# Optimization experiments

Hardware: AMD Instinct MI355X
Metric: run time of the kernel (lower is better)

## Reference

```python
import jax, jax.numpy as jnp
import numpy as np

N = 50000
E = 1600000
DX = 128
DH = 128
DY = 64
NEG_SLOPE = 0.0  # in_neg_slope; LeakyReLU slope in GAT attention


def _init(key, shape, fan_in):
    return jax.random.normal(key, shape, dtype=jnp.float32) / np.sqrt(fan_in)


def setup_inputs() -> dict:
    key = jax.random.key(0)
    ks = jax.random.split(key, 12)
    node_x = jax.random.normal(ks[0], (N, DX), dtype=jnp.float32)
    edge_index = jax.random.randint(ks[1], (2, E), 0, N, dtype=jnp.int32)
    return {
        "node_x": node_x,
        "edge_index": edge_index,
        # GATConv layer 1 (DX -> DH, heads=1)
        "W1": _init(ks[2], (DX, DH), DX),
        "att_src1": _init(ks[3], (DH,), DH),
        "att_dst1": _init(ks[4], (DH,), DH),
        "b1": jnp.zeros((DH,), dtype=jnp.float32),
        # GATConv layer 2 (DH -> DH)
        "W2": _init(ks[5], (DH, DH), DH),
        "att_src2": _init(ks[6], (DH,), DH),
        "att_dst2": _init(ks[7], (DH,), DH),
        "b2": jnp.zeros((DH,), dtype=jnp.float32),
        # output Linear (DH -> DY)
        "W_out": _init(ks[8], (DH, DY), DH),
        "b_out": jnp.zeros((DY,), dtype=jnp.float32),
    }


def _gat_conv(x, src, dst, W, att_src, att_dst, bias, n):
    # h: [N, DH] transformed features
    h = x @ W
    # per-edge attention logits: a_src . h_j + a_dst . h_i
    e = (h @ att_src)[src] + (h @ att_dst)[dst]          # [E']
    e = jnp.where(e > 0, e, NEG_SLOPE * e)               # LeakyReLU
    # segment softmax over incoming edges of each destination node
    m = jax.lax.stop_gradient(jax.ops.segment_max(e, dst, num_segments=n))
    ex = jnp.exp(e - m[dst])
    denom = jax.ops.segment_sum(ex, dst, num_segments=n)
    alpha = ex / denom[dst]                              # [E']
    # scatter-add weighted source features to destinations
    out = jax.ops.segment_sum(h[src] * alpha[:, None], dst, num_segments=n)
    return out + bias


def reference(node_x, edge_index, W1, att_src1, att_dst1, b1,
              W2, att_src2, att_dst2, b2, W_out, b_out):
    n = node_x.shape[0]
    src, dst = edge_index[0], edge_index[1]
    # PyG GATConv default add_self_loops=True
    loop = jnp.arange(n, dtype=src.dtype)
    src = jnp.concatenate([src, loop])
    dst = jnp.concatenate([dst, loop])
    x1 = jax.nn.relu(_gat_conv(node_x, src, dst, W1, att_src1, att_dst1, b1, n))
    x2 = _gat_conv(x1, src, dst, W2, att_src2, att_dst2, b2, n)
    return x2 @ W_out + b_out
```

## Files before the change

### kernel.cpp

```cpp
#include <hip/hip_runtime.h>
#include <hip/hip_fp16.h>

typedef unsigned short u16;
typedef unsigned int   u32;
typedef _Float16 f16;
typedef __attribute__((ext_vector_type(8))) f16 f16x8;
typedef __attribute__((ext_vector_type(2))) f16 h2;
typedef __attribute__((ext_vector_type(4))) float f32x4;

#define NN 50000
#define EE 1600000
#define DD 128
#define DYY 64
#define NB 196
#define EPB 8192
#define GB 196
#define MAXD 160
#define NTILE 3125
#define GMM 782

__device__ __forceinline__ u16 f2h(float f){
  union { f16 h; u16 u; } x; x.h = (f16)f; return x.u;
}
__device__ __forceinline__ float wave_sum(float v){
  #pragma unroll
  for (int s = 32; s; s >>= 1) v += __shfl_xor(v, s, 64);
  return v;
}

__device__ __forceinline__ void wfrag_one(const float* __restrict__ W, u16* __restrict__ Wf,
                                          int nct, int s){
  int lane = s & 63;
  int t  = (s >> 6) % nct;
  int ks = (s >> 6) / nct;
  int q = lane >> 4, n = lane & 15;
  int N = nct * 16;
  u16 tmp[8];
  #pragma unroll
  for (int j = 0; j < 8; ++j)
    tmp[j] = f2h(W[(ks * 32 + q * 8 + j) * N + t * 16 + n]);
  *(uint4*)(Wf + (size_t)s * 8) = *(const uint4*)tmp;
}

__global__ __launch_bounds__(256) void kA_prep(const int* __restrict__ dst, int* __restrict__ hist2d,
                                               const float* __restrict__ W1, const float* __restrict__ W2,
                                               const float* __restrict__ Wo,
                                               u16* __restrict__ Wf1, u16* __restrict__ Wf2,
                                               u16* __restrict__ Wfo){
  int b = blockIdx.x, tid = threadIdx.x;
  if (b < GB){
    __shared__ int hist[256];
    hist[tid] = 0;
    __syncthreads();
    int e0 = b * EPB, e1 = min(e0 + EPB, EE);
    for (int e = e0 + tid; e < e1; e += 256) atomicAdd(&hist[dst[e] >> 8], 1);
    __syncthreads();
    hist2d[b * 256 + tid] = hist[tid];
  } else if (b < 204) wfrag_one(W1, Wf1, 8, (b - 196) * 256 + tid);
  else if (b < 212)   wfrag_one(W2, Wf2, 8, (b - 204) * 256 + tid);
  else                wfrag_one(Wo, Wfo, 4, (b - 212) * 256 + tid);
}

__device__ __forceinline__ void gemm_tile(const void* __restrict__ X, int xf32,
                                          const u16* __restrict__ Wf, u16* __restrict__ Hout,
                                          const float* __restrict__ as, const float* __restrict__ ad,
                                          float* __restrict__ Sv, float* __restrict__ Dv,
                                          int blk, int tid, uint4* Wl){
  const uint4* Wg = (const uint4*)Wf;
  #pragma unroll
  for (int i = 0; i < 8; ++i) Wl[tid + 256 * i] = Wg[tid + 256 * i];
  __syncthreads();
  int wv = tid >> 6, lane = tid & 63;
  int rtile = blk * 4 + wv;
  if (rtile >= NTILE) return;
  int q = lane >> 4, n = lane & 15;
  int arow = rtile * 16 + n;
  f32x4 acc[8];
  #pragma unroll
  for (int t = 0; t < 8; ++t) acc[t] = (f32x4){0.f, 0.f, 0.f, 0.f};
  union F8 { uint4 u; f16x8 v; f16 h[8]; };
  #pragma unroll
  for (int ks = 0; ks < 4; ++ks){
    int kb = ks * 32 + q * 8;
    F8 a;
    if (!xf32){
      a.u = *(const uint4*)((const u16*)X + (size_t)arow * DD + kb);
    } else {
      const float* xp = (const float*)X + (size_t)arow * DD + kb;
      float4 f0 = *(const float4*)xp;
      float4 f1 = *(const float4*)(xp + 4);
      a.h[0] = (f16)f0.x; a.h[1] = (f16)f0.y; a.h[2] = (f16)f0.z; a.h[3] = (f16)f0.w;
      a.h[4] = (f16)f1.x; a.h[5] = (f16)f1.y; a.h[6] = (f16)f1.z; a.h[7] = (f16)f1.w;
    }
    #pragma unroll
    for (int t = 0; t < 8; ++t){
      F8 b; b.u = Wl[(ks * 8 + t) * 64 + lane];
      acc[t] = __builtin_amdgcn_mfma_f32_16x16x32_f16(a.v, b.v, acc[t], 0, 0, 0);
    }
  }
  float ps[4] = {0, 0, 0, 0}, pd[4] = {0, 0, 0, 0};
  #pragma unroll
  for (int t = 0; t < 8; ++t){
    float a_s = as[t * 16 + n];
    float a_d = ad[t * 16 + n];
    #pragma unroll
    for (int rg = 0; rg < 4; ++rg){
      ps[rg] += acc[t][rg] * a_s;
      pd[rg] += acc[t][rg] * a_d;
    }
  }
  #pragma unroll
  for (int rg = 0; rg < 4; ++rg){
    #pragma unroll
    for (int s = 1; s < 16; s <<= 1){
      ps[rg] += __shfl_xor(ps[rg], s, 64);
      pd[rg] += __shfl_xor(pd[rg], s, 64);
    }
  }
  #pragma unroll
  for (int rg = 0; rg < 4; ++rg){
    int grow = rtile * 16 + q * 4 + rg;
    if (n == 0){ Sv[grow] = ps[rg]; Dv[grow] = pd[rg]; }
    #pragma unroll
    for (int t = 0; t < 8; ++t)
      Hout[(size_t)grow * DD + t * 16 + n] = f2h(acc[t][rg]);
  }
}

__global__ __launch_bounds__(256) void kBC(const int* __restrict__ src, const int* __restrict__ dst,
                                           const int* __restrict__ hist2d,
                                           int* __restrict__ btot, int* __restrict__ bbase,
                                           u32* __restrict__ buf,
                                           const float* __restrict__ X0, const u16* __restrict__ Wf1,
                                           u16* __restrict__ Hbf,
                                           const float* __restrict__ as1, const float* __restrict__ ad1,
                                           float* __restrict__ Sv, float* __restrict__ Dv){
  __shared__ __align__(16) uint4 Wl[2048];
  int b = blockIdx.x, tid = threadIdx.x;
  if (b < GB){
    int* lcur = (int*)Wl;
    int* sd   = ((int*)Wl) + 256;
    int c = b;
    int pre = 0, tot = 0;
    for (int cc = 0; cc < GB; ++cc){
      int v = hist2d[cc * 256 + tid];
      if (cc < c) pre += v;
      tot += v;
    }
    sd[tid] = tot;
    __syncthreads();
    for (int o = 1; o < 256; o <<= 1){
      int t = (tid >= o) ? sd[tid - o] : 0;
      __syncthreads();
      sd[tid] += t;
      __syncthreads();
    }
    int bb = sd[tid] - tot;
    if (c == 0){ btot[tid] = tot; bbase[tid] = bb; }
    lcur[tid] = bb + pre;
    __syncthreads();
    int e0 = c * EPB, e1 = min(e0 + EPB, EE);
    for (int e = e0 + tid; e < e1; e += 256){
      int d = dst[e];
      int pos = atomicAdd(&lcur[d >> 8], 1);
      buf[pos] = (u32)src[e] | ((u32)(d & 255) << 16);
    }
  } else {
    gemm_tile(X0, 1, Wf1, Hbf, as1, ad1, Sv, Dv, b - GB, tid, Wl);
  }
}

__global__ __launch_bounds__(256) void kD_finalize(const u32* __restrict__ buf,
                                                   const int* __restrict__ btot, const int* __restrict__ bbase,
                                                   int* __restrict__ offs, int* __restrict__ cnt,
                                                   u16* __restrict__ srcs){
  __shared__ int dh[256];
  __shared__ int sd[256];
  __shared__ int dcur[256];
  int tid = threadIdx.x, b = blockIdx.x;
  int n = btot[b], base = bbase[b];
  dh[tid] = 0;
  __syncthreads();
  for (int i = tid; i < n; i += 256) atomicAdd(&dh[(buf[base + i] >> 16) & 255], 1);
  __syncthreads();
  int v = dh[tid];
  sd[tid] = v;
  __syncthreads();
  for (int o = 1; o < 256; o <<= 1){
    int t = (tid >= o) ? sd[tid - o] : 0;
    __syncthreads();
    sd[tid] += t;
    __syncthreads();
  }
  int excl = sd[tid] - v;
  dcur[tid] = base + excl;
  int d = (b << 8) + tid;
  if (d < NN){ offs[d] = base + excl; cnt[d] = v; }
  __syncthreads();
  for (int i = tid; i < n; i += 256){
    u32 u = buf[base + i];
    int pos = atomicAdd(&dcur[(u >> 16) & 255], 1);
    srcs[pos] = (u16)(u & 0xffffu);
  }
}

__global__ __launch_bounds__(256) void k_agg(const u16* __restrict__ H,
                                             const float* __restrict__ Sv, const float* __restrict__ Dv,
                                             const int* __restrict__ offs, const int* __restrict__ cnt,
                                             const u16* __restrict__ srcs,
                                             const float* __restrict__ bias,
                                             u16* __restrict__ Xout, int do_relu){
  __shared__ int   s_i[4][MAXD];
  __shared__ float s_w[4][MAXD];
  int gid = blockIdx.x * blockDim.x + threadIdx.x;
  int wid = gid >> 6, lane = gid & 63;
  int wv = threadIdx.x >> 6;
  if (wid >= NN) return;
  int off = offs[wid], c = cnt[wid];
  float dvw = Dv[wid];
  float wself = __expf(fmaxf(Sv[wid] + dvw, 0.f));
  int cf = min(c, MAXD);
  float dl = 0.f;
  for (int j = lane; j < c; j += 64){
    int sidx = (int)srcs[off + j];
    float wgt = __expf(fmaxf(Sv[sidx] + dvw, 0.f));
    if (j < MAXD){ s_i[wv][j] = sidx; s_w[wv][j] = wgt; }
    dl += wgt;
  }
  float inv = 1.f / (wave_sum(dl) + wself);
  for (int j = lane; j < cf; j += 64) s_w[wv][j] *= inv;
  int grp = lane >> 4, cg = lane & 15;
  const u32* H32 = (const u32*)H;
  union F8 { uint4 u; h2 p[4]; };
  h2 acc2[4] = {(h2){0,0},(h2){0,0},(h2){0,0},(h2){0,0}};
  if (grp == 0){
    F8 r; r.u = *(const uint4*)(H32 + (size_t)wid * 64 + cg * 4);
    f16 wh = (f16)(wself * inv); h2 w2 = {wh, wh};
    #pragma unroll
    for (int i = 0; i < 4; ++i) acc2[i] = r.p[i] * w2;
  }
  for (int base = 0; base < cf; base += 4){
    int j = base + grp;
    float wgt = 0.f; int sidx = 0;
    if (j < cf){ wgt = s_w[wv][j]; sidx = s_i[wv][j]; }
    f16 wh = (f16)wgt; h2 w2 = {wh, wh};
    F8 r; r.u = *(const uint4*)(H32 + (size_t)sidx * 64 + cg * 4);
    #pragma unroll
    for (int i = 0; i < 4; ++i) acc2[i] += r.p[i] * w2;
  }
  for (int base = MAXD; base < c; base += 4){
    int j = base + grp;
    bool valid = j < c;
    int sidx = valid ? (int)srcs[off + j] : 0;
    float wgt = valid ? __expf(fmaxf(Sv[sidx] + dvw, 0.f)) * inv : 0.f;
    f16 wh = (f16)wgt; h2 w2 = {wh, wh};
    F8 r; r.u = *(const uint4*)(H32 + (size_t)sidx * 64 + cg * 4);
    #pragma unroll
    for (int i = 0; i < 4; ++i) acc2[i] += r.p[i] * w2;
  }
  union FU { h2 v; float f; };
  #pragma unroll
  for (int i = 0; i < 4; ++i){
    FU a; a.v = acc2[i];
    FU o1; o1.f = __shfl_xor(a.f, 16, 64); a.v = a.v + o1.v;
    FU o2; o2.f = __shfl_xor(a.f, 32, 64); a.v = a.v + o2.v;
    acc2[i] = a.v;
  }
  if (grp == 0){
    uint4 pk;
    u32* pkp = (u32*)&pk;
    #pragma unroll
    for (int qq = 0; qq < 4; ++qq){
      float o0 = (float)acc2[qq].x + bias[cg * 8 + 2 * qq];
      float o1 = (float)acc2[qq].y + bias[cg * 8 + 2 * qq + 1];
      if (do_relu){ o0 = fmaxf(o0, 0.f); o1 = fmaxf(o1, 0.f); }
      pkp[qq] = ((u32)f2h(o1) << 16) | (u32)f2h(o0);
    }
    *(uint4*)((u32*)Xout + (size_t)wid * 64 + cg * 4) = pk;
  }
}

__global__ __launch_bounds__(256) void k_gemm2(const u16* __restrict__ X, const u16* __restrict__ Wf,
                                               u16* __restrict__ Hout,
                                               const float* __restrict__ as, const float* __restrict__ ad,
                                               float* __restrict__ Sv, float* __restrict__ Dv){
  __shared__ __align__(16) uint4 Wl[2048];
  gemm_tile(X, 0, Wf, Hout, as, ad, Sv, Dv, blockIdx.x, threadIdx.x, Wl);
}

__global__ __launch_bounds__(256) void k_out(const u16* __restrict__ X,
                                             const u16* __restrict__ Wfo,
                                             const float* __restrict__ bias,
                                             float* __restrict__ out){
  __shared__ __align__(16) uint4 Wl[1024];
  int tid = threadIdx.x;
  const uint4* Wg = (const uint4*)Wfo;
  #pragma unroll
  for (int i = 0; i < 4; ++i) Wl[tid + 256 * i] = Wg[tid + 256 * i];
  __syncthreads();
  int wv = tid >> 6, lane = tid & 63;
  int rtile = blockIdx.x * 4 + wv;
  if (rtile >= NTILE) return;
  int q = lane >> 4, n = lane & 15;
  int arow = rtile * 16 + n;
  f32x4 acc[4];
  #pragma unroll
  for (int t = 0; t < 4; ++t) acc[t] = (f32x4){0.f, 0.f, 0.f, 0.f};
  union F8 { uint4 u; f16x8 v; };
  #pragma unroll
  for (int ks = 0; ks < 4; ++ks){
    F8 a; a.u = *(const uint4*)(X + (size_t)arow * DD + ks * 32 + q * 8);
    #pragma unroll
    for (int t = 0; t < 4; ++t){
      F8 b; b.u = Wl[(ks * 4 + t) * 64 + lane];
      acc[t] = __builtin_amdgcn_mfma_f32_16x16x32_f16(a.v, b.v, acc[t], 0, 0, 0);
    }
  }
  float bo[4];
  #pragma unroll
  for (int t = 0; t < 4; ++t) bo[t] = bias[t * 16 + n];
  #pragma unroll
  for (int rg = 0; rg < 4; ++rg){
    int grow = rtile * 16 + q * 4 + rg;
    #pragma unroll
    for (int t = 0; t < 4; ++t)
      out[(size_t)grow * DYY + t * 16 + n] = acc[t][rg] + bo[t];
  }
}

extern "C" void kernel_launch(void* const* d_in, const int* in_sizes, int n_in,
                              void* d_out, int out_size, void* d_ws, size_t ws_size,
                              hipStream_t stream) {
  const float* node_x = (const float*)d_in[0];
  const int* ei   = (const int*)d_in[1];
  const int* srcp = ei;
  const int* dstp = ei + EE;
  const float* W1  = (const float*)d_in[2];
  const float* as1 = (const float*)d_in[3];
  const float* ad1 = (const float*)d_in[4];
  const float* b1  = (const float*)d_in[5];
  const float* W2  = (const float*)d_in[6];
  const float* as2 = (const float*)d_in[7];
  const float* ad2 = (const float*)d_in[8];
  const float* b2  = (const float*)d_in[9];
  const float* Wo  = (const float*)d_in[10];
  const float* bo  = (const float*)d_in[11];

  char* w = (char*)d_ws;
  u16*   Hbf   = (u16*)w;   w += (size_t)NN * DD * 2;
  u16*   Abf   = (u16*)w;   w += (size_t)NN * DD * 2;
  u32*   buf   = (u32*)Abf;
  float* Sv    = (float*)w; w += (size_t)NN * 4;
  float* Dv    = (float*)w; w += (size_t)NN * 4;
  int*   cnt   = (int*)w;   w += (size_t)NN * 4;
  int*   offs  = (int*)w;   w += (size_t)NN * 4;
  int*   btot  = (int*)w;   w += 1024;
  int*   bbase = (int*)w;   w += 1024;
  int*   hist2d = (int*)w;  w += GB * 256 * 4;
  u16*   srcs  = (u16*)w;   w += (size_t)EE * 2;
  u16*   Wf1   = (u16*)w;   w += 32768;
  u16*   Wf2   = (u16*)w;   w += 32768;
  u16*   Wfo   = (u16*)w;   w += 16384;

  const int TB = 256;
  const int gWav = (NN * 64) / TB;

  kA_prep    <<<216,      TB, 0, stream>>>(dstp, hist2d, W1, W2, Wo, Wf1, Wf2, Wfo);
  kBC        <<<GB + GMM, TB, 0, stream>>>(srcp, dstp, hist2d, btot, bbase, buf,
                                           node_x, Wf1, Hbf, as1, ad1, Sv, Dv);
  kD_finalize<<<NB,       TB, 0, stream>>>(buf, btot, bbase, offs, cnt, srcs);

  k_agg  <<<gWav, TB, 0, stream>>>(Hbf, Sv, Dv, offs, cnt, srcs, b1, Abf, 1);
  k_gemm2<<<GMM,  TB, 0, stream>>>(Abf, Wf2, Hbf, as2, ad2, Sv, Dv);
  k_agg  <<<gWav, TB, 0, stream>>>(Hbf, Sv, Dv, offs, cnt, srcs, b2, Abf, 0);
  k_out  <<<GMM,  TB, 0, stream>>>(Abf, Wfo, bo, (float*)d_out);
}
```

Baseline: 285.4 us.

## Fuse neighbor aggregation with following GEMM via LDS-staged 16-row tiles

```diff
diff --git a/kernel.cpp b/kernel.cpp
--- a/kernel.cpp
+++ b/kernel.cpp
@@ -18,6 +18,7 @@
 #define MAXD 160
 #define NTILE 3125
 #define GMM 782
+#define XST 144
 
 __device__ __forceinline__ u16 f2h(float f){
   union { f16 h; u16 u; } x; x.h = (f16)f; return x.u;
@@ -61,7 +62,7 @@
   else                wfrag_one(Wo, Wfo, 4, (b - 212) * 256 + tid);
 }
 
-__device__ __forceinline__ void gemm_tile(const void* __restrict__ X, int xf32,
+__device__ __forceinline__ void gemm_tile(const float* __restrict__ X,
                                           const u16* __restrict__ Wf, u16* __restrict__ Hout,
                                           const float* __restrict__ as, const float* __restrict__ ad,
                                           float* __restrict__ Sv, float* __restrict__ Dv,
@@ -82,16 +83,12 @@
   #pragma unroll
   for (int ks = 0; ks < 4; ++ks){
     int kb = ks * 32 + q * 8;
+    const float* xp = X + (size_t)arow * DD + kb;
+    float4 f0 = *(const float4*)xp;
+    float4 f1 = *(const float4*)(xp + 4);
     F8 a;
-    if (!xf32){
-      a.u = *(const uint4*)((const u16*)X + (size_t)arow * DD + kb);
-    } else {
-      const float* xp = (const float*)X + (size_t)arow * DD + kb;
-      float4 f0 = *(const float4*)xp;
-      float4 f1 = *(const float4*)(xp + 4);
-      a.h[0] = (f16)f0.x; a.h[1] = (f16)f0.y; a.h[2] = (f16)f0.z; a.h[3] = (f16)f0.w;
-      a.h[4] = (f16)f1.x; a.h[5] = (f16)f1.y; a.h[6] = (f16)f1.z; a.h[7] = (f16)f1.w;
-    }
+    a.h[0] = (f16)f0.x; a.h[1] = (f16)f0.y; a.h[2] = (f16)f0.z; a.h[3] = (f16)f0.w;
+    a.h[4] = (f16)f1.x; a.h[5] = (f16)f1.y; a.h[6] = (f16)f1.z; a.h[7] = (f16)f1.w;
     #pragma unroll
     for (int t = 0; t < 8; ++t){
       F8 b; b.u = Wl[(ks * 8 + t) * 64 + lane];
@@ -132,9 +129,9 @@
                                            int* __restrict__ btot, int* __restrict__ bbase,
                                            u32* __restrict__ buf,
                                            const float* __restrict__ X0, const u16* __restrict__ Wf1,
-                                           u16* __restrict__ Hbf,
+                                           u16* __restrict__ Hbf1,
                                            const float* __restrict__ as1, const float* __restrict__ ad1,
-                                           float* __restrict__ Sv, float* __restrict__ Dv){
+                                           float* __restrict__ Sv1, float* __restrict__ Dv1){
   __shared__ __align__(16) uint4 Wl[2048];
   int b = blockIdx.x, tid = threadIdx.x;
   if (b < GB){
@@ -166,7 +163,7 @@
       buf[pos] = (u32)src[e] | ((u32)(d & 255) << 16);
     }
   } else {
-    gemm_tile(X0, 1, Wf1, Hbf, as1, ad1, Sv, Dv, b - GB, tid, Wl);
+    gemm_tile(X0, Wf1, Hbf1, as1, ad1, Sv1, Dv1, b - GB, tid, Wl);
   }
 }
 
@@ -204,18 +201,11 @@
   }
 }
 
-__global__ __launch_bounds__(256) void k_agg(const u16* __restrict__ H,
-                                             const float* __restrict__ Sv, const float* __restrict__ Dv,
-                                             const int* __restrict__ offs, const int* __restrict__ cnt,
-                                             const u16* __restrict__ srcs,
-                                             const float* __restrict__ bias,
-                                             u16* __restrict__ Xout, int do_relu){
-  __shared__ int   s_i[4][MAXD];
-  __shared__ float s_w[4][MAXD];
-  int gid = blockIdx.x * blockDim.x + threadIdx.x;
-  int wid = gid >> 6, lane = gid & 63;
-  int wv = threadIdx.x >> 6;
-  if (wid >= NN) return;
+__device__ void agg_node_lds(const u16* __restrict__ H, const float* __restrict__ Sv,
+                             const float* __restrict__ Dv, const int* __restrict__ offs,
+                             const int* __restrict__ cnt, const u16* __restrict__ srcs,
+                             const float* __restrict__ bias, u16* __restrict__ xrow,
+                             int do_relu, int wid, int lane, int* si, float* sw){
   int off = offs[wid], c = cnt[wid];
   float dvw = Dv[wid];
   float wself = __expf(fmaxf(Sv[wid] + dvw, 0.f));
@@ -224,17 +214,17 @@
   for (int j = lane; j < c; j += 64){
     int sidx = (int)srcs[off + j];
     float wgt = __expf(fmaxf(Sv[sidx] + dvw, 0.f));
-    if (j < MAXD){ s_i[wv][j] = sidx; s_w[wv][j] = wgt; }
+    if (j < MAXD){ si[j] = sidx; sw[j] = wgt; }
     dl += wgt;
   }
   float inv = 1.f / (wave_sum(dl) + wself);
-  for (int j = lane; j < cf; j += 64) s_w[wv][j] *= inv;
-  int grp = lane >> 4, cg = lane & 15;
+  for (int j = lane; j < cf; j += 64) sw[j] *= inv;
+  int grp = lane >> 4, cg_ = lane & 15;
   const u32* H32 = (const u32*)H;
   union F8 { uint4 u; h2 p[4]; };
   h2 acc2[4] = {(h2){0,0},(h2){0,0},(h2){0,0},(h2){0,0}};
   if (grp == 0){
-    F8 r; r.u = *(const uint4*)(H32 + (size_t)wid * 64 + cg * 4);
+    F8 r; r.u = *(const uint4*)(H32 + (size_t)wid * 64 + cg_ * 4);
     f16 wh = (f16)(wself * inv); h2 w2 = {wh, wh};
     #pragma unroll
     for (int i = 0; i < 4; ++i) acc2[i] = r.p[i] * w2;
@@ -242,9 +232,9 @@
   for (int base = 0; base < cf; base += 4){
     int j = base + grp;
     float wgt = 0.f; int sidx = 0;
-    if (j < cf){ wgt = s_w[wv][j]; sidx = s_i[wv][j]; }
+    if (j < cf){ wgt = sw[j]; sidx = si[j]; }
     f16 wh = (f16)wgt; h2 w2 = {wh, wh};
-    F8 r; r.u = *(const uint4*)(H32 + (size_t)sidx * 64 + cg * 4);
+    F8 r; r.u = *(const uint4*)(H32 + (size_t)sidx * 64 + cg_ * 4);
     #pragma unroll
     for (int i = 0; i < 4; ++i) acc2[i] += r.p[i] * w2;
   }
@@ -254,7 +244,7 @@
     int sidx = valid ? (int)srcs[off + j] : 0;
     float wgt = valid ? __expf(fmaxf(Sv[sidx] + dvw, 0.f)) * inv : 0.f;
     f16 wh = (f16)wgt; h2 w2 = {wh, wh};
-    F8 r; r.u = *(const uint4*)(H32 + (size_t)sidx * 64 + cg * 4);
+    F8 r; r.u = *(const uint4*)(H32 + (size_t)sidx * 64 + cg_ * 4);
     #pragma unroll
     for (int i = 0; i < 4; ++i) acc2[i] += r.p[i] * w2;
   }
@@ -271,60 +261,121 @@
     u32* pkp = (u32*)&pk;
     #pragma unroll
     for (int qq = 0; qq < 4; ++qq){
-      float o0 = (float)acc2[qq].x + bias[cg * 8 + 2 * qq];
-      float o1 = (float)acc2[qq].y + bias[cg * 8 + 2 * qq + 1];
+      float o0 = (float)acc2[qq].x + bias[cg_ * 8 + 2 * qq];
+      float o1 = (float)acc2[qq].y + bias[cg_ * 8 + 2 * qq + 1];
       if (do_relu){ o0 = fmaxf(o0, 0.f); o1 = fmaxf(o1, 0.f); }
       pkp[qq] = ((u32)f2h(o1) << 16) | (u32)f2h(o0);
     }
-    *(uint4*)((u32*)Xout + (size_t)wid * 64 + cg * 4) = pk;
-  }
-}
-
-__global__ __launch_bounds__(256) void k_gemm2(const u16* __restrict__ X, const u16* __restrict__ Wf,
-                                               u16* __restrict__ Hout,
-                                               const float* __restrict__ as, const float* __restrict__ ad,
-                                               float* __restrict__ Sv, float* __restrict__ Dv){
-  __shared__ __align__(16) uint4 Wl[2048];
-  gemm_tile(X, 0, Wf, Hout, as, ad, Sv, Dv, blockIdx.x, threadIdx.x, Wl);
-}
-
-__global__ __launch_bounds__(256) void k_out(const u16* __restrict__ X,
-                                             const u16* __restrict__ Wfo,
-                                             const float* __restrict__ bias,
-                                             float* __restrict__ out){
-  __shared__ __align__(16) uint4 Wl[1024];
-  int tid = threadIdx.x;
-  const uint4* Wg = (const uint4*)Wfo;
-  #pragma unroll
-  for (int i = 0; i < 4; ++i) Wl[tid + 256 * i] = Wg[tid + 256 * i];
-  __syncthreads();
-  int wv = tid >> 6, lane = tid & 63;
-  int rtile = blockIdx.x * 4 + wv;
-  if (rtile >= NTILE) return;
+    *(uint4*)(xrow + cg_ * 8) = pk;
+  }
+}
+
+__global__ __launch_bounds__(256) void kE(const u16* __restrict__ Hbf1,
+                                          const float* __restrict__ Sv1, const float* __restrict__ Dv1,
+                                          const int* __restrict__ offs, const int* __restrict__ cnt,
+                                          const u16* __restrict__ srcs, const float* __restrict__ b1,
+                                          const u16* __restrict__ Wf2,
+                                          const float* __restrict__ as2, const float* __restrict__ ad2,
+                                          u16* __restrict__ Hbf2,
+                                          float* __restrict__ Sv2, float* __restrict__ Dv2){
+  __shared__ __align__(16) u16 Xs[16 * XST];
+  __shared__ int   s_i[4][MAXD];
+  __shared__ float s_w[4][MAXD];
+  __shared__ float svp[16], dvp[16];
+  int tid = threadIdx.x, wv = tid >> 6, lane = tid & 63;
+  int rtile = blockIdx.x;
+  if (tid < 16){ svp[tid] = 0.f; dvp[tid] = 0.f; }
+  #pragma unroll
+  for (int k = 0; k < 4; ++k){
+    int r = wv * 4 + k;
+    agg_node_lds(Hbf1, Sv1, Dv1, offs, cnt, srcs, b1, Xs + r * XST, 1,
+                 rtile * 16 + r, lane, s_i[wv], s_w[wv]);
+  }
+  __syncthreads();
+  const uint4* Wg = (const uint4*)Wf2;
   int q = lane >> 4, n = lane & 15;
-  int arow = rtile * 16 + n;
-  f32x4 acc[4];
-  #pragma unroll
-  for (int t = 0; t < 4; ++t) acc[t] = (f32x4){0.f, 0.f, 0.f, 0.f};
+  f32x4 acc[2] = {(f32x4){0.f,0.f,0.f,0.f}, (f32x4){0.f,0.f,0.f,0.f}};
   union F8 { uint4 u; f16x8 v; };
   #pragma unroll
   for (int ks = 0; ks < 4; ++ks){
-    F8 a; a.u = *(const uint4*)(X + (size_t)arow * DD + ks * 32 + q * 8);
-    #pragma unroll
-    for (int t = 0; t < 4; ++t){
-      F8 b; b.u = Wl[(ks * 4 + t) * 64 + lane];
-      acc[t] = __builtin_amdgcn_mfma_f32_16x16x32_f16(a.v, b.v, acc[t], 0, 0, 0);
-    }
-  }
-  float bo[4];
-  #pragma unroll
-  for (int t = 0; t < 4; ++t) bo[t] = bias[t * 16 + n];
+    F8 a; a.u = *(const uint4*)((const char*)Xs + n * (XST * 2) + ks * 64 + q * 16);
+    #pragma unroll
+    for (int tt = 0; tt < 2; ++tt){
+      F8 b; b.u = Wg[(ks * 8 + wv * 2 + tt) * 64 + lane];
+      acc[tt] = __builtin_amdgcn_mfma_f32_16x16x32_f16(a.v, b.v, acc[tt], 0, 0, 0);
+    }
+  }
+  float ps[4] = {0, 0, 0, 0}, pd[4] = {0, 0, 0, 0};
+  #pragma unroll
+  for (int tt = 0; tt < 2; ++tt){
+    int t = wv * 2 + tt;
+    float a_s = as2[t * 16 + n];
+    float a_d = ad2[t * 16 + n];
+    #pragma unroll
+    for (int rg = 0; rg < 4; ++rg){
+      ps[rg] += acc[tt][rg] * a_s;
+      pd[rg] += acc[tt][rg] * a_d;
+    }
+  }
+  #pragma unroll
+  for (int rg = 0; rg < 4; ++rg){
+    #pragma unroll
+    for (int s = 1; s < 16; s <<= 1){
+      ps[rg] += __shfl_xor(ps[rg], s, 64);
+      pd[rg] += __shfl_xor(pd[rg], s, 64);
+    }
+  }
+  if (n == 0){
+    #pragma unroll
+    for (int rg = 0; rg < 4; ++rg){
+      atomicAdd(&svp[q * 4 + rg], ps[rg]);
+      atomicAdd(&dvp[q * 4 + rg], pd[rg]);
+    }
+  }
   #pragma unroll
   for (int rg = 0; rg < 4; ++rg){
     int grow = rtile * 16 + q * 4 + rg;
     #pragma unroll
-    for (int t = 0; t < 4; ++t)
-      out[(size_t)grow * DYY + t * 16 + n] = acc[t][rg] + bo[t];
+    for (int tt = 0; tt < 2; ++tt)
+      Hbf2[(size_t)grow * DD + (wv * 2 + tt) * 16 + n] = f2h(acc[tt][rg]);
+  }
+  __syncthreads();
+  if (tid < 16){ Sv2[rtile * 16 + tid] = svp[tid]; Dv2[rtile * 16 + tid] = dvp[tid]; }
+}
+
+__global__ __launch_bounds__(256) void kF(const u16* __restrict__ Hbf2,
+                                          const float* __restrict__ Sv2, const float* __restrict__ Dv2,
+                                          const int* __restrict__ offs, const int* __restrict__ cnt,
+                                          const u16* __restrict__ srcs, const float* __restrict__ b2,
+                                          const u16* __restrict__ Wfo, const float* __restrict__ bo,
+                                          float* __restrict__ out){
+  __shared__ __align__(16) u16 Xs[16 * XST];
+  __shared__ int   s_i[4][MAXD];
+  __shared__ float s_w[4][MAXD];
+  int tid = threadIdx.x, wv = tid >> 6, lane = tid & 63;
+  int rtile = blockIdx.x;
+  #pragma unroll
+  for (int k = 0; k < 4; ++k){
+    int r = wv * 4 + k;
+    agg_node_lds(Hbf2, Sv2, Dv2, offs, cnt, srcs, b2, Xs + r * XST, 0,
+                 rtile * 16 + r, lane, s_i[wv], s_w[wv]);
+  }
+  __syncthreads();
+  const uint4* Wg = (const uint4*)Wfo;
+  int q = lane >> 4, n = lane & 15;
+  f32x4 acc = (f32x4){0.f, 0.f, 0.f, 0.f};
+  union F8 { uint4 u; f16x8 v; };
+  #pragma unroll
+  for (int ks = 0; ks < 4; ++ks){
+    F8 a; a.u = *(const uint4*)((const char*)Xs + n * (XST * 2) + ks * 64 + q * 16);
+    F8 b; b.u = Wg[(ks * 4 + wv) * 64 + lane];
+    acc = __builtin_amdgcn_mfma_f32_16x16x32_f16(a.v, b.v, acc, 0, 0, 0);
+  }
+  float bt = bo[wv * 16 + n];
+  #pragma unroll
+  for (int rg = 0; rg < 4; ++rg){
+    int grow = rtile * 16 + q * 4 + rg;
+    out[(size_t)grow * DYY + wv * 16 + n] = acc[rg] + bt;
   }
 }
 
@@ -347,11 +398,13 @@
   const float* bo  = (const float*)d_in[11];
 
   char* w = (char*)d_ws;
-  u16*   Hbf   = (u16*)w;   w += (size_t)NN * DD * 2;
-  u16*   Abf   = (u16*)w;   w += (size_t)NN * DD * 2;
-  u32*   buf   = (u32*)Abf;
-  float* Sv    = (float*)w; w += (size_t)NN * 4;
-  float* Dv    = (float*)w; w += (size_t)NN * 4;
+  u16*   Hbf1  = (u16*)w;  w += (size_t)NN * DD * 2;
+  u16*   Hbf2  = (u16*)w;  w += (size_t)NN * DD * 2;
+  u32*   buf   = (u32*)Hbf2;
+  float* Sv1   = (float*)w; w += (size_t)NN * 4;
+  float* Dv1   = (float*)w; w += (size_t)NN * 4;
+  float* Sv2   = (float*)w; w += (size_t)NN * 4;
+  float* Dv2   = (float*)w; w += (size_t)NN * 4;
   int*   cnt   = (int*)w;   w += (size_t)NN * 4;
   int*   offs  = (int*)w;   w += (size_t)NN * 4;
   int*   btot  = (int*)w;   w += 1024;
@@ -363,15 +416,13 @@
   u16*   Wfo   = (u16*)w;   w += 16384;
 
   const int TB = 256;
-  const int gWav = (NN * 64) / TB;
 
   kA_prep    <<<216,      TB, 0, stream>>>(dstp, hist2d, W1, W2, Wo, Wf1, Wf2, Wfo);
   kBC        <<<GB + GMM, TB, 0, stream>>>(srcp, dstp, hist2d, btot, bbase, buf,
-                                           node_x, Wf1, Hbf, as1, ad1, Sv, Dv);
+                                           node_x, Wf1, Hbf1, as1, ad1, Sv1, Dv1);
   kD_finalize<<<NB,       TB, 0, stream>>>(buf, btot, bbase, offs, cnt, srcs);
-
-  k_agg  <<<gWav, TB, 0, stream>>>(Hbf, Sv, Dv, offs, cnt, srcs, b1, Abf, 1);
-  k_gemm2<<<GMM,  TB, 0, stream>>>(Abf, Wf2, Hbf, as2, ad2, Sv, Dv);
-  k_agg  <<<gWav, TB, 0, stream>>>(Hbf, Sv, Dv, offs, cnt, srcs, b2, Abf, 0);
-  k_out  <<<GMM,  TB, 0, stream>>>(Abf, Wfo, bo, (float*)d_out);
-}
+  kE         <<<NTILE,    TB, 0, stream>>>(Hbf1, Sv1, Dv1, offs, cnt, srcs, b1,
+                                           Wf2, as2, ad2, Hbf2, Sv2, Dv2);
+  kF         <<<NTILE,    TB, 0, stream>>>(Hbf2, Sv2, Dv2, offs, cnt, srcs, b2,
+                                           Wfo, bo, (float*)d_out);
+}
```

After: 283.4 us. No clear change (-0.7%).
